# Kernel tuning notes

Measured on AMD Instinct MI355X. Metric: run time of the kernel, lower is better.

The kernel has to match this reference:

```python
import jax, jax.numpy as jnp
import numpy as np

N_HEAD = 12
N_EMBED = 768

def setup_inputs() -> dict:
    key = jax.random.key(0)
    ks = jax.random.split(key, 5)
    B, T, C = 8, 1024, N_EMBED
    s_in = 1.0 / np.sqrt(C)
    s3 = 1.0 / np.sqrt(3 * C)
    return {
        "x": jax.random.normal(ks[0], (B, T, C), dtype=jnp.float32),
        "W_qkv": jax.random.normal(ks[1], (C, 3 * C), dtype=jnp.float32) * s_in,
        "b_qkv": jnp.zeros((3 * C,), dtype=jnp.float32),
        "W_out": jax.random.normal(ks[2], (C, C), dtype=jnp.float32) * s_in,
        "b_out": jnp.zeros((C,), dtype=jnp.float32),
    }

def reference(x, W_qkv, b_qkv, W_out, b_out):
    B, T, C = x.shape
    H = N_HEAD
    d_k = C // H
    qkv = x @ W_qkv + b_qkv  # [B,T,3C]
    q, k, v = jnp.split(qkv, 3, axis=-1)
    # [B,H,T,d]
    q = q.reshape(B, T, H, d_k).transpose(0, 2, 1, 3)
    k = k.reshape(B, T, H, d_k).transpose(0, 2, 1, 3)
    v = v.reshape(B, T, H, d_k).transpose(0, 2, 1, 3)
    logits = jnp.einsum('bhqd,bhkd->bhqk', q, k) * (d_k ** -0.5)
    causal = jnp.tril(jnp.ones((T, T), dtype=bool))
    logits = jnp.where(causal, logits, -jnp.inf)
    scores = jax.nn.softmax(logits, axis=-1)
    out = jnp.einsum('bhqk,bhkd->bhqd', scores, v)
    out = out.transpose(0, 2, 1, 3).reshape(B, T, C)
    return out @ W_out + b_out
```

## Files before the change

kernel.cpp:

```cpp
#include <hip/hip_runtime.h>
#include <stdint.h>

#define B_ 8
#define T_ 1024
#define C_ 768
#define H_ 12
#define DK 64
#define BT (B_*T_)
#define NQKV (3*C_)

typedef unsigned short u16;
typedef __bf16 bf16x8 __attribute__((ext_vector_type(8)));
typedef __bf16 bf16x4 __attribute__((ext_vector_type(4)));
typedef float  f32x4  __attribute__((ext_vector_type(4)));

typedef const __attribute__((address_space(1))) void gvoid_t;
typedef __attribute__((address_space(3))) void lvoid_t;

#define SBARRIER()  asm volatile("s_barrier" ::: "memory")
#define SWAITCNT(s) asm volatile("s_waitcnt " s ::: "memory")

__device__ __forceinline__ void gl_lds16(const void* g, void* l) {
    __builtin_amdgcn_global_load_lds((gvoid_t*)g, (lvoid_t*)l, 16, 0, 0);
}

__device__ __forceinline__ u16 f2b(float f) {
    union { float f; unsigned int u; } v; v.f = f;
    unsigned int u = v.u;
    return (u16)((u + 0x7fffu + ((u >> 16) & 1u)) >> 16);
}

__device__ __forceinline__ f32x4 mfma16(bf16x8 a, bf16x8 b, f32x4 c) {
    return __builtin_amdgcn_mfma_f32_16x16x32_bf16(a, b, c, 0, 0, 0);
}

__global__ __launch_bounds__(256)
void k_prep(const float* __restrict__ x, u16* __restrict__ xb,
            const float* __restrict__ wqkv, u16* __restrict__ wqkvT,
            const float* __restrict__ wout, u16* __restrict__ woutT)
{
    __shared__ u16 tile[32][34];
    const int bid = blockIdx.x;
    const int tid = threadIdx.x;
    if (bid < 6144) {
        int i = bid * 256 + tid;
        float4 f = ((const float4*)x)[i];
        uint2 o;
        o.x = (unsigned)f2b(f.x) | ((unsigned)f2b(f.y) << 16);
        o.y = (unsigned)f2b(f.z) | ((unsigned)f2b(f.w) << 16);
        ((uint2*)xb)[i] = o;
        return;
    }
    const float* w; u16* wt; int K, N, n0, k0;
    if (bid < 6144 + 1728) {
        int idx = bid - 6144;
        w = wqkv; wt = wqkvT; K = C_; N = NQKV;
        n0 = (idx % 72) * 32; k0 = (idx / 72) * 32;
    } else {
        int idx = bid - 7872;
        w = wout; wt = woutT; K = C_; N = C_;
        n0 = (idx % 24) * 32; k0 = (idx / 24) * 32;
    }
    const int tx = tid & 31, ty = tid >> 5;
    #pragma unroll
    for (int i = 0; i < 4; i++)
        tile[ty + i * 8][tx] = f2b(w[(size_t)(k0 + ty + i * 8) * N + n0 + tx]);
    __syncthreads();
    #pragma unroll
    for (int i = 0; i < 4; i++)
        wt[(size_t)(n0 + ty + i * 8) * K + k0 + tx] = tile[tx][ty + i * 8];
}

__global__ __launch_bounds__(256, 3)
void k_gemm_qkv(const u16* __restrict__ A, const u16* __restrict__ Bt,
                const float* __restrict__ bias,
                u16* __restrict__ qo, u16* __restrict__ ko, u16* __restrict__ vto)
{
    const int K = C_;
    __shared__ u16 As[3][128 * 32];
    __shared__ u16 Bs[3][96 * 32];
    const int tid  = threadIdx.x;
    const int lane = tid & 63;
    const int w    = tid >> 6;
    const int quad = lane >> 4;
    const int col  = lane & 15;

    const int id   = blockIdx.x + gridDim.x * blockIdx.y;
    const int xcd  = id & 7;
    const int slot = id >> 3;
    const int m0   = (xcd * 8 + (slot & 7)) * 128;
    const int n0   = (slot >> 3) * 96;

    const int wm   = (w >> 1) * 64;
    const int wn   = (w & 1) * 48;

    f32x4 zero4 = {0.f, 0.f, 0.f, 0.f};
    f32x4 acc[4][3];
    #pragma unroll
    for (int i = 0; i < 4; i++)
        #pragma unroll
        for (int j = 0; j < 3; j++) acc[i][j] = zero4;

    const int sr  = tid >> 2;
    const int scc = ((tid & 3) ^ ((sr >> 1) & 3)) * 8;
    const u16* gA = A  + (size_t)(m0 + sr) * K + scc;
    const u16* gB = Bt + (size_t)(n0 + sr) * K + scc;

    const int NIT = K >> 5;

    #define STAGE(kt, bufi)                                                          \
        do {                                                                         \
            gl_lds16(gA + (kt),                  (char*)As[bufi] + w * 1024);        \
            gl_lds16(gA + (size_t)64 * K + (kt), (char*)As[bufi] + 4096 + w * 1024); \
            gl_lds16(gB + (kt),                  (char*)Bs[bufi] + w * 1024);        \
            if (w < 2)                                                               \
                gl_lds16(gB + (size_t)64 * K + (kt), (char*)Bs[bufi] + 4096 + w * 1024); \
        } while (0)

    STAGE(0, 0);
    STAGE(32, 1);
    int cur = 0;
    for (int it = 0; it < NIT; ++it) {
        if (it + 1 < NIT) {
            if (w < 2) { SWAITCNT("vmcnt(4)"); } else { SWAITCNT("vmcnt(3)"); }
        } else {
            SWAITCNT("vmcnt(0)");
        }
        SBARRIER();
        if (it + 2 < NIT) {
            int b2 = cur + 2; if (b2 >= 3) b2 -= 3;
            STAGE((it + 2) << 5, b2);
        }

        const u16* Ab = As[cur];
        const u16* Bb = Bs[cur];
        bf16x8 af[4], bfr[3];
        #pragma unroll
        for (int mt = 0; mt < 4; mt++) {
            int row = wm + mt * 16 + col;
            af[mt] = *(const bf16x8*)&Ab[row * 32 + ((quad ^ ((row >> 1) & 3)) * 8)];
        }
        #pragma unroll
        for (int nt = 0; nt < 3; nt++) {
            int row = wn + nt * 16 + col;
            bfr[nt] = *(const bf16x8*)&Bb[row * 32 + ((quad ^ ((row >> 1) & 3)) * 8)];
        }
        #pragma unroll
        for (int mt = 0; mt < 4; mt++)
            #pragma unroll
            for (int nt = 0; nt < 3; nt++)
                acc[mt][nt] = mfma16(af[mt], bfr[nt], acc[mt][nt]);

        cur = (cur == 2) ? 0 : cur + 1;
    }
    #undef STAGE

    #pragma unroll
    for (int mt = 0; mt < 4; mt++) {
        #pragma unroll
        for (int nt = 0; nt < 3; nt++) {
            #pragma unroll
            for (int r = 0; r < 4; r++) {
                int m = m0 + wm + mt * 16 + quad * 4 + r;
                int n = n0 + wn + nt * 16 + col;
                float v = acc[mt][nt][r] + bias[n];
                int sec = n / C_;
                int c   = n - sec * C_;
                int h   = c >> 6;
                int d   = c & 63;
                int b   = m >> 10;
                int t   = m & 1023;
                int bh  = b * H_ + h;
                u16 bv  = f2b(v);
                if (sec == 0)      qo [((size_t)bh * T_ + t) * DK + d] = bv;
                else if (sec == 1) ko [((size_t)bh * T_ + t) * DK + d] = bv;
                else               vto[((size_t)bh * DK + d) * T_ + t] = bv;
            }
        }
    }
}

__global__ __launch_bounds__(256, 4)
void k_gemm_out(const u16* __restrict__ A, const u16* __restrict__ Bt,
                const float* __restrict__ bias, float* __restrict__ outf)
{
    const int K = C_, N = C_;
    __shared__ u16 As[3][128 * 32];
    __shared__ u16 Bs[3][64 * 32];
    const int tid  = threadIdx.x;
    const int lane = tid & 63;
    const int w    = tid >> 6;
    const int quad = lane >> 4;
    const int col  = lane & 15;

    const int id   = blockIdx.x;
    const int xcd  = id & 7;
    const int slot = id >> 3;
    const int m0   = (xcd * 8 + (slot & 7)) * 128;
    const int n0   = (slot >> 3) * 64;

    f32x4 zero4 = {0.f, 0.f, 0.f, 0.f};
    f32x4 acc[2][4];
    #pragma unroll
    for (int i = 0; i < 2; i++)
        #pragma unroll
        for (int j = 0; j < 4; j++) acc[i][j] = zero4;

    const int sr  = tid >> 2;
    const int scc = ((tid & 3) ^ ((sr >> 1) & 3)) * 8;
    const u16* gA = A  + (size_t)(m0 + sr) * K + scc;
    const u16* gB = Bt + (size_t)(n0 + sr) * K + scc;

    const int NIT = K >> 5;

    #define STAGE(kt, bufi)                                                          \
        do {                                                                         \
            gl_lds16(gA + (kt),                  (char*)As[bufi] + w * 1024);        \
            gl_lds16(gA + (size_t)64 * K + (kt), (char*)As[bufi] + 4096 + w * 1024); \
            gl_lds16(gB + (kt),                  (char*)Bs[bufi] + w * 1024);        \
        } while (0)

    STAGE(0, 0);
    STAGE(32, 1);
    int cur = 0;
    for (int it = 0; it < NIT; ++it) {
        if (it + 1 < NIT) {
            SWAITCNT("vmcnt(3)");
        } else {
            SWAITCNT("vmcnt(0)");
        }
        SBARRIER();
        if (it + 2 < NIT) {
            int b2 = cur + 2; if (b2 >= 3) b2 -= 3;
            STAGE((it + 2) << 5, b2);
        }

        const u16* Ab = As[cur];
        const u16* Bb = Bs[cur];
        bf16x8 af[2], bfr[4];
        #pragma unroll
        for (int mt = 0; mt < 2; mt++) {
            int row = w * 32 + mt * 16 + col;
            af[mt] = *(const bf16x8*)&Ab[row * 32 + ((quad ^ ((row >> 1) & 3)) * 8)];
        }
        #pragma unroll
        for (int nt = 0; nt < 4; nt++) {
            int row = nt * 16 + col;
            bfr[nt] = *(const bf16x8*)&Bb[row * 32 + ((quad ^ ((row >> 1) & 3)) * 8)];
        }
        #pragma unroll
        for (int mt = 0; mt < 2; mt++)
            #pragma unroll
            for (int nt = 0; nt < 4; nt++)
                acc[mt][nt] = mfma16(af[mt], bfr[nt], acc[mt][nt]);

        cur = (cur == 2) ? 0 : cur + 1;
    }
    #undef STAGE

    #pragma unroll
    for (int mt = 0; mt < 2; mt++) {
        #pragma unroll
        for (int nt = 0; nt < 4; nt++) {
            #pragma unroll
            for (int r = 0; r < 4; r++) {
                int m = m0 + w * 32 + mt * 16 + quad * 4 + r;
                int n = n0 + nt * 16 + col;
                outf[(size_t)m * N + n] = acc[mt][nt][r] + bias[n];
            }
        }
    }
}

#define PSTRIDE 72

__device__ __forceinline__ bf16x8 ld_sw(const u16* base, int row, int half,
                                        int quad, int c7) {
    return *(const bf16x8*)(base + row * DK + (((half * 4 + quad) ^ c7) * 8));
}

template <bool MASK>
__device__ __forceinline__ void attn_chunk(
    const u16* Ks, const u16* Vs, __bf16* pbuf,
    const bf16x8 (&qf)[2][2], bf16x8 ones,
    int kv0, int qw, int quad, int col,
    f32x4 (&oacc)[2][4], f32x4 (&lacc)[2])
{
    const int c7 = col & 7;
    f32x4 zero4 = {0.f, 0.f, 0.f, 0.f};
    f32x4 st[2][4];
    #pragma unroll
    for (int g = 0; g < 4; g++) {
        bf16x8 klo = ld_sw(Ks, g * 16 + col, 0, quad, c7);
        bf16x8 khi = ld_sw(Ks, g * 16 + col, 1, quad, c7);
        st[0][g] = mfma16(khi, qf[0][1], mfma16(klo, qf[0][0], zero4));
        st[1][g] = mfma16(khi, qf[1][1], mfma16(klo, qf[1][0], zero4));
    }
    const float scl = 0.18033688f;
    #pragma unroll
    for (int s = 0; s < 2; s++) {
        __bf16* pb = pbuf + s * 16 * PSTRIDE + col * PSTRIDE;
        #pragma unroll
        for (int g = 0; g < 4; g++) {
            bf16x4 pp;
            #pragma unroll
            for (int r = 0; r < 4; r++) {
                float p = __builtin_amdgcn_exp2f(st[s][g][r] * scl - 12.0f);
                if (MASK) {
                    int kv = kv0 + g * 16 + quad * 4 + r;
                    if (kv > qw + s * 16 + col) p = 0.f;
                }
                pp[r] = (__bf16)p;
            }
            *(bf16x4*)(pb + g * 16 + quad * 4) = pp;
        }
    }
    SWAITCNT("lgkmcnt(0)");
    bf16x8 pf[2][2];
    #pragma unroll
    for (int s = 0; s < 2; s++) {
        const __bf16* pb = pbuf + s * 16 * PSTRIDE + col * PSTRIDE;
        pf[s][0] = *(const bf16x8*)(pb + quad * 8);
        pf[s][1] = *(const bf16x8*)(pb + 32 + quad * 8);
        lacc[s] = mfma16(pf[s][1], ones, mfma16(pf[s][0], ones, lacc[s]));
    }
    #pragma unroll
    for (int dt = 0; dt < 4; dt++) {
        bf16x8 vlo = ld_sw(Vs, dt * 16 + col, 0, quad, c7);
        bf16x8 vhi = ld_sw(Vs, dt * 16 + col, 1, quad, c7);
        #pragma unroll
        for (int s = 0; s < 2; s++)
            oacc[s][dt] = mfma16(pf[s][1], vhi, mfma16(pf[s][0], vlo, oacc[s][dt]));
    }
}

__global__ __launch_bounds__(256, 3)
void k_attn(const u16* __restrict__ Q, const u16* __restrict__ Kf,
            const u16* __restrict__ Vt, u16* __restrict__ Of)
{
    __shared__ u16 Ks[2][64 * DK];
    __shared__ u16 Vs[2][64 * DK];
    __shared__ __bf16 Plds[4][32 * PSTRIDE];
    const int bh   = blockIdx.x;
    const int b    = bh / H_;
    const int h    = bh - b * H_;
    const int tid  = threadIdx.x;
    const int lane = tid & 63;
    const int w    = tid >> 6;
    const int quad = lane >> 4;
    const int col  = lane & 15;
    const int ty   = 7 - (int)blockIdx.y;
    const int nch  = 2 * ty + 2;
    const int qw   = ty * 128 + w * 32;
    __bf16* pbuf = Plds[w];

    const u16* Qb = Q  + (size_t)bh * T_ * DK;
    const u16* Kb = Kf + (size_t)bh * T_ * DK;
    const u16* Vb = Vt + (size_t)bh * DK * T_;

    int sG0 = tid, sG1 = 256 + tid;
    int sr0 = sG0 >> 3, sg0 = (sG0 & 7) ^ (sr0 & 7);
    int sr1 = sG1 >> 3, sg1 = (sG1 & 7) ^ (sr1 & 7);

    bf16x8 qf[2][2];
    #pragma unroll
    for (int s = 0; s < 2; s++) {
        const u16* qp = Qb + (size_t)(qw + s * 16 + col) * DK;
        qf[s][0] = *(const bf16x8*)(qp + quad * 8);
        qf[s][1] = *(const bf16x8*)(qp + 32 + quad * 8);
    }

    bf16x8 ones;
    #pragma unroll
    for (int i = 0; i < 8; i++) ((u16*)&ones)[i] = 0x3F80;

    f32x4 zero4 = {0.f, 0.f, 0.f, 0.f};
    f32x4 oacc[2][4];
    f32x4 lacc[2] = {zero4, zero4};
    #pragma unroll
    for (int s = 0; s < 2; s++)
        #pragma unroll
        for (int dt = 0; dt < 4; dt++) oacc[s][dt] = zero4;

    #define ASTAGE(c, bufi)                                                            \
        do {                                                                           \
            int kvs = (c) * 64;                                                        \
            gl_lds16(Kb + (size_t)(kvs + sr0) * DK + sg0 * 8, (char*)Ks[bufi] + w * 1024);        \
            gl_lds16(Kb + (size_t)(kvs + sr1) * DK + sg1 * 8, (char*)Ks[bufi] + 4096 + w * 1024); \
            gl_lds16(Vb + (size_t)sr0 * T_ + kvs + sg0 * 8,   (char*)Vs[bufi] + w * 1024);        \
            gl_lds16(Vb + (size_t)sr1 * T_ + kvs + sg1 * 8,   (char*)Vs[bufi] + 4096 + w * 1024); \
        } while (0)

    ASTAGE(0, 0);
    #pragma unroll 1
    for (int c = 0; c < nch; ++c) {
        const int cur = c & 1;
        SWAITCNT("vmcnt(0)");
        SBARRIER();
        if (c + 1 < nch) {
            ASTAGE(c + 1, cur ^ 1);
        }

        const int kv0 = c * 64;
        if (kv0 <= qw + 31) {
            if (kv0 + 63 <= qw)
                attn_chunk<false>(Ks[cur], Vs[cur], pbuf, qf, ones, kv0, qw, quad, col, oacc, lacc);
            else
                attn_chunk<true>(Ks[cur], Vs[cur], pbuf, qf, ones, kv0, qw, quad, col, oacc, lacc);
        }
    }
    #undef ASTAGE

    #pragma unroll
    for (int s = 0; s < 2; s++) {
        #pragma unroll
        for (int r = 0; r < 4; r++) {
            float inv = 1.f / lacc[s][r];
            int t = qw + s * 16 + quad * 4 + r;
            u16* op = Of + ((size_t)(b * T_ + t)) * C_ + h * DK;
            #pragma unroll
            for (int dt = 0; dt < 4; dt++) op[dt * 16 + col] = f2b(oacc[s][dt][r] * inv);
        }
    }
}

extern "C" void kernel_launch(void* const* d_in, const int* in_sizes, int n_in,
                              void* d_out, int out_size, void* d_ws, size_t ws_size,
                              hipStream_t stream) {
    const float* x    = (const float*)d_in[0];
    const float* Wqkv = (const float*)d_in[1];
    const float* bqkv = (const float*)d_in[2];
    const float* Wout = (const float*)d_in[3];
    const float* bout = (const float*)d_in[4];
    float* out = (float*)d_out;

    char* ws = (char*)d_ws;
    u16* xb    = (u16*)(ws);
    u16* wqkvT = (u16*)(ws + 12582912);
    u16* woutT = (u16*)(ws + 16121856);
    u16* qw    = (u16*)(ws + 17301504);
    u16* kw    = (u16*)(ws + 29884416);
    u16* vtw   = (u16*)(ws + 42467328);
    u16* aw    = (u16*)(ws + 55050240);

    k_prep<<<8448, 256, 0, stream>>>(x, xb, Wqkv, wqkvT, Wout, woutT);

    k_gemm_qkv<<<dim3(NQKV / 96, BT / 128), 256, 0, stream>>>(
        xb, wqkvT, bqkv, qw, kw, vtw);

    k_attn<<<dim3(B_ * H_, 8), 256, 0, stream>>>(qw, kw, vtw, aw);

    k_gemm_out<<<768, 256, 0, stream>>>(aw, woutT, bout, out);
}
```

Measured before the change: 181.4 us.

## Switch QKV GEMM to double-buffered 64-wide K stages

Replaces the 3-deep ring of 32-wide K tiles in the QKV projection GEMM with a 2-deep double buffer of 64-wide K stages. Each stage holds two 32-wide sub-tiles, and each iteration runs twice as many MFMAs. This halves the number of barrier and wait rounds per block, but every iteration now waits for all outstanding loads (vmcnt(0)), so prefetch depth shrinks to one stage. The larger LDS footprint also lowers the occupancy hint from 3 to 2 blocks per CU.

```diff
diff --git a/kernel.cpp b/kernel.cpp
--- a/kernel.cpp
+++ b/kernel.cpp
@@ -71,14 +71,14 @@
         wt[(size_t)(n0 + ty + i * 8) * K + k0 + tx] = tile[tx][ty + i * 8];
 }
 
-__global__ __launch_bounds__(256, 3)
+__global__ __launch_bounds__(256, 2)
 void k_gemm_qkv(const u16* __restrict__ A, const u16* __restrict__ Bt,
                 const float* __restrict__ bias,
                 u16* __restrict__ qo, u16* __restrict__ ko, u16* __restrict__ vto)
 {
     const int K = C_;
-    __shared__ u16 As[3][128 * 32];
-    __shared__ u16 Bs[3][96 * 32];
+    __shared__ u16 As[2][2][128 * 32];
+    __shared__ u16 Bs[2][2][96 * 32];
     const int tid  = threadIdx.x;
     const int lane = tid & 63;
     const int w    = tid >> 6;
@@ -106,54 +106,50 @@
     const u16* gA = A  + (size_t)(m0 + sr) * K + scc;
     const u16* gB = Bt + (size_t)(n0 + sr) * K + scc;
 
-    const int NIT = K >> 5;
-
-    #define STAGE(kt, bufi)                                                          \
-        do {                                                                         \
-            gl_lds16(gA + (kt),                  (char*)As[bufi] + w * 1024);        \
-            gl_lds16(gA + (size_t)64 * K + (kt), (char*)As[bufi] + 4096 + w * 1024); \
-            gl_lds16(gB + (kt),                  (char*)Bs[bufi] + w * 1024);        \
-            if (w < 2)                                                               \
-                gl_lds16(gB + (size_t)64 * K + (kt), (char*)Bs[bufi] + 4096 + w * 1024); \
+    const int NT64 = K >> 6;
+
+    #define SUB(kt, bufi, subi)                                                           \
+        do {                                                                              \
+            gl_lds16(gA + (kt),                  (char*)As[bufi][subi] + w * 1024);       \
+            gl_lds16(gA + (size_t)64 * K + (kt), (char*)As[bufi][subi] + 4096 + w * 1024);\
+            gl_lds16(gB + (kt),                  (char*)Bs[bufi][subi] + w * 1024);       \
+            if (w < 2)                                                                    \
+                gl_lds16(gB + (size_t)64 * K + (kt), (char*)Bs[bufi][subi] + 4096 + w * 1024);\
         } while (0)
+    #define STAGE(t, bufi)  do { SUB(((t) << 6), bufi, 0); SUB(((t) << 6) + 32, bufi, 1); } while (0)
 
     STAGE(0, 0);
-    STAGE(32, 1);
-    int cur = 0;
-    for (int it = 0; it < NIT; ++it) {
-        if (it + 1 < NIT) {
-            if (w < 2) { SWAITCNT("vmcnt(4)"); } else { SWAITCNT("vmcnt(3)"); }
-        } else {
-            SWAITCNT("vmcnt(0)");
-        }
+    for (int it = 0; it < NT64; ++it) {
+        const int cur = it & 1;
+        SWAITCNT("vmcnt(0)");
         SBARRIER();
-        if (it + 2 < NIT) {
-            int b2 = cur + 2; if (b2 >= 3) b2 -= 3;
-            STAGE((it + 2) << 5, b2);
-        }
-
-        const u16* Ab = As[cur];
-        const u16* Bb = Bs[cur];
-        bf16x8 af[4], bfr[3];
-        #pragma unroll
-        for (int mt = 0; mt < 4; mt++) {
-            int row = wm + mt * 16 + col;
-            af[mt] = *(const bf16x8*)&Ab[row * 32 + ((quad ^ ((row >> 1) & 3)) * 8)];
-        }
-        #pragma unroll
-        for (int nt = 0; nt < 3; nt++) {
-            int row = wn + nt * 16 + col;
-            bfr[nt] = *(const bf16x8*)&Bb[row * 32 + ((quad ^ ((row >> 1) & 3)) * 8)];
-        }
-        #pragma unroll
-        for (int mt = 0; mt < 4; mt++)
-            #pragma unroll
-            for (int nt = 0; nt < 3; nt++)
-                acc[mt][nt] = mfma16(af[mt], bfr[nt], acc[mt][nt]);
-
-        cur = (cur == 2) ? 0 : cur + 1;
+        if (it + 1 < NT64)
+            STAGE(it + 1, cur ^ 1);
+
+        #pragma unroll
+        for (int kk = 0; kk < 2; ++kk) {
+            const u16* Ab = As[cur][kk];
+            const u16* Bb = Bs[cur][kk];
+            bf16x8 af[4], bfr[3];
+            #pragma unroll
+            for (int mt = 0; mt < 4; mt++) {
+                int row = wm + mt * 16 + col;
+                af[mt] = *(const bf16x8*)&Ab[row * 32 + ((quad ^ ((row >> 1) & 3)) * 8)];
+            }
+            #pragma unroll
+            for (int nt = 0; nt < 3; nt++) {
+                int row = wn + nt * 16 + col;
+                bfr[nt] = *(const bf16x8*)&Bb[row * 32 + ((quad ^ ((row >> 1) & 3)) * 8)];
+            }
+            #pragma unroll
+            for (int mt = 0; mt < 4; mt++)
+                #pragma unroll
+                for (int nt = 0; nt < 3; nt++)
+                    acc[mt][nt] = mfma16(af[mt], bfr[nt], acc[mt][nt]);
+        }
     }
     #undef STAGE
+    #undef SUB
 
     #pragma unroll
     for (int mt = 0; mt < 4; mt++) {
```

Result: no change. 181.9 us (+0.2%).

## Widen QKV GEMM tile to cover matching Q, K, V column slices per block

Applied to the files above, without the earlier changes.

Each QKV GEMM block now computes a 128x288 tile made of three 96-column slices, one each from the Q, K and V sections at the same offset. The grid shrinks from 24x64 to 8x64, so each A tile is loaded once for three times as many output columns. Each wave covers 32 rows by 288 columns with 36 accumulators. Occupancy drops to 2 blocks per CU, register pressure and LDS use go up, and there are fewer blocks to spread across the GPU.

```diff
diff --git a/kernel.cpp b/kernel.cpp
--- a/kernel.cpp
+++ b/kernel.cpp
@@ -71,14 +71,14 @@
         wt[(size_t)(n0 + ty + i * 8) * K + k0 + tx] = tile[tx][ty + i * 8];
 }
 
-__global__ __launch_bounds__(256, 3)
+__global__ __launch_bounds__(256, 2)
 void k_gemm_qkv(const u16* __restrict__ A, const u16* __restrict__ Bt,
                 const float* __restrict__ bias,
                 u16* __restrict__ qo, u16* __restrict__ ko, u16* __restrict__ vto)
 {
     const int K = C_;
     __shared__ u16 As[3][128 * 32];
-    __shared__ u16 Bs[3][96 * 32];
+    __shared__ u16 Bs[3][288 * 32];
     const int tid  = threadIdx.x;
     const int lane = tid & 63;
     const int w    = tid >> 6;
@@ -91,15 +91,14 @@
     const int m0   = (xcd * 8 + (slot & 7)) * 128;
     const int n0   = (slot >> 3) * 96;
 
-    const int wm   = (w >> 1) * 64;
-    const int wn   = (w & 1) * 48;
+    const int wm   = w * 32;
 
     f32x4 zero4 = {0.f, 0.f, 0.f, 0.f};
-    f32x4 acc[4][3];
-    #pragma unroll
-    for (int i = 0; i < 4; i++)
-        #pragma unroll
-        for (int j = 0; j < 3; j++) acc[i][j] = zero4;
+    f32x4 acc[2][18];
+    #pragma unroll
+    for (int i = 0; i < 2; i++)
+        #pragma unroll
+        for (int j = 0; j < 18; j++) acc[i][j] = zero4;
 
     const int sr  = tid >> 2;
     const int scc = ((tid & 3) ^ ((sr >> 1) & 3)) * 8;
@@ -108,13 +107,18 @@
 
     const int NIT = K >> 5;
 
-    #define STAGE(kt, bufi)                                                          \
-        do {                                                                         \
-            gl_lds16(gA + (kt),                  (char*)As[bufi] + w * 1024);        \
-            gl_lds16(gA + (size_t)64 * K + (kt), (char*)As[bufi] + 4096 + w * 1024); \
-            gl_lds16(gB + (kt),                  (char*)Bs[bufi] + w * 1024);        \
-            if (w < 2)                                                               \
-                gl_lds16(gB + (size_t)64 * K + (kt), (char*)Bs[bufi] + 4096 + w * 1024); \
+    #define STAGE(kt, bufi)                                                               \
+        do {                                                                              \
+            gl_lds16(gA + (kt),                  (char*)As[bufi] + w * 1024);             \
+            gl_lds16(gA + (size_t)64 * K + (kt), (char*)As[bufi] + 4096 + w * 1024);      \
+            _Pragma("unroll")                                                             \
+            for (int s = 0; s < 3; s++) {                                                 \
+                const u16* gBs = gB + (size_t)(s * C_) * K;                               \
+                gl_lds16(gBs + (kt), (char*)Bs[bufi] + s * 6144 + w * 1024);              \
+                if (w < 2)                                                                \
+                    gl_lds16(gBs + (size_t)64 * K + (kt),                                 \
+                             (char*)Bs[bufi] + s * 6144 + 4096 + w * 1024);               \
+            }                                                                             \
         } while (0)
 
     STAGE(0, 0);
@@ -122,7 +126,7 @@
     int cur = 0;
     for (int it = 0; it < NIT; ++it) {
         if (it + 1 < NIT) {
-            if (w < 2) { SWAITCNT("vmcnt(4)"); } else { SWAITCNT("vmcnt(3)"); }
+            if (w < 2) { SWAITCNT("vmcnt(8)"); } else { SWAITCNT("vmcnt(5)"); }
         } else {
             SWAITCNT("vmcnt(0)");
         }
@@ -134,44 +138,40 @@
 
         const u16* Ab = As[cur];
         const u16* Bb = Bs[cur];
-        bf16x8 af[4], bfr[3];
-        #pragma unroll
-        for (int mt = 0; mt < 4; mt++) {
+        bf16x8 af[2];
+        #pragma unroll
+        for (int mt = 0; mt < 2; mt++) {
             int row = wm + mt * 16 + col;
             af[mt] = *(const bf16x8*)&Ab[row * 32 + ((quad ^ ((row >> 1) & 3)) * 8)];
         }
         #pragma unroll
-        for (int nt = 0; nt < 3; nt++) {
-            int row = wn + nt * 16 + col;
-            bfr[nt] = *(const bf16x8*)&Bb[row * 32 + ((quad ^ ((row >> 1) & 3)) * 8)];
-        }
-        #pragma unroll
-        for (int mt = 0; mt < 4; mt++)
-            #pragma unroll
-            for (int nt = 0; nt < 3; nt++)
-                acc[mt][nt] = mfma16(af[mt], bfr[nt], acc[mt][nt]);
+        for (int nt = 0; nt < 18; nt++) {
+            int row = nt * 16 + col;
+            bf16x8 bfr = *(const bf16x8*)&Bb[row * 32 + ((quad ^ ((row >> 1) & 3)) * 8)];
+            acc[0][nt] = mfma16(af[0], bfr, acc[0][nt]);
+            acc[1][nt] = mfma16(af[1], bfr, acc[1][nt]);
+        }
 
         cur = (cur == 2) ? 0 : cur + 1;
     }
     #undef STAGE
 
     #pragma unroll
-    for (int mt = 0; mt < 4; mt++) {
-        #pragma unroll
-        for (int nt = 0; nt < 3; nt++) {
+    for (int mt = 0; mt < 2; mt++) {
+        #pragma unroll
+        for (int nt = 0; nt < 18; nt++) {
+            const int sec = nt / 6;
+            const int cc  = n0 + (nt - sec * 6) * 16 + col;
+            const int h   = cc >> 6;
+            const int d   = cc & 63;
             #pragma unroll
             for (int r = 0; r < 4; r++) {
                 int m = m0 + wm + mt * 16 + quad * 4 + r;
-                int n = n0 + wn + nt * 16 + col;
-                float v = acc[mt][nt][r] + bias[n];
-                int sec = n / C_;
-                int c   = n - sec * C_;
-                int h   = c >> 6;
-                int d   = c & 63;
-                int b   = m >> 10;
-                int t   = m & 1023;
-                int bh  = b * H_ + h;
-                u16 bv  = f2b(v);
+                int b = m >> 10;
+                int t = m & 1023;
+                int bh = b * H_ + h;
+                float v = acc[mt][nt][r] + bias[sec * C_ + cc];
+                u16 bv = f2b(v);
                 if (sec == 0)      qo [((size_t)bh * T_ + t) * DK + d] = bv;
                 else if (sec == 1) ko [((size_t)bh * T_ + t) * DK + d] = bv;
                 else               vto[((size_t)bh * DK + d) * T_ + t] = bv;
@@ -445,7 +445,7 @@
 
     k_prep<<<8448, 256, 0, stream>>>(x, xb, Wqkv, wqkvT, Wout, woutT);
 
-    k_gemm_qkv<<<dim3(NQKV / 96, BT / 128), 256, 0, stream>>>(
+    k_gemm_qkv<<<dim3(8, BT / 128), 256, 0, stream>>>(
         xb, wqkvT, bqkv, qw, kw, vtw);
 
     k_attn<<<dim3(B_ * H_, 8), 256, 0, stream>>>(qw, kw, vtw, aw);
```

Result: faster. 175.7 us (-3.1%).
